# Kernel optimization log

Hardware: AMD Instinct MI355X
Metric: run time of the kernel (lower is better)

Reference implementation:

```python
import jax, jax.numpy as jnp
import numpy as np

N_VARS = 16
BATCH = 16
SEQ = 512
P = N_VARS * (N_VARS - 1)  # ordered pairs i != j


def setup_inputs() -> dict:
    key = jax.random.key(0)
    ks = jax.random.split(key, 12)
    n = N_VARS

    def w(k, shape, fan_in):
        return jax.random.normal(k, shape, dtype=jnp.float32) / np.sqrt(fan_in)

    z = lambda *s: jnp.zeros(s, jnp.float32)
    return {
        'data': jax.random.normal(ks[0], (BATCH, SEQ, n), dtype=jnp.float32),
        # structure learner: n*n -> 256 -> 128 -> n*n (dropout skipped / eval mode)
        'Ws1': w(ks[1], (n * n, 256), n * n), 'bs1': z(256),
        'Ws2': w(ks[2], (256, 128), 256), 'bs2': z(128),
        'Ws3': w(ks[3], (128, n * n), 128), 'bs3': z(n * n),
        # per-variable causal mechanisms (stacked): (n-1) -> 128 -> 64 -> 1
        'Wm1': w(ks[4], (n, n - 1, 128), n - 1), 'bm1': z(n, 128),
        'Wm2': w(ks[5], (n, 128, 64), 128), 'bm2': z(n, 64),
        'Wm3': w(ks[6], (n, 64), 64), 'bm3': z(n),
        # per-pair independence tests (stacked): 2 -> 32 -> 1, sigmoid
        'Wt1': w(ks[7], (P, 2, 32), 2), 'bt1': z(P, 32),
        'Wt2': w(ks[8], (P, 32), 32), 'bt2': z(P),
    }


def reference(data, Ws1, bs1, Ws2, bs2, Ws3, bs3,
              Wm1, bm1, Wm2, bm2, Wm3, bm3,
              Wt1, bt1, Wt2, bt2):
    B, S, n = data.shape
    N = B * S
    flat = data.reshape(N, n)  # [N, n] all samples

    # ---- correlations of batch-averaged series (vectorized corrcoef) ----
    avg = data.mean(axis=0)                    # [S, n]
    xc = avg - avg.mean(axis=0, keepdims=True)
    cov = xc.T @ xc                            # [n, n]
    std = jnp.sqrt(jnp.clip(jnp.diag(cov), 0.0))
    denom = std[:, None] * std[None, :]
    corr = jnp.abs(jnp.where(denom > 0, cov / jnp.where(denom > 0, denom, 1.0), 0.0))
    corr = corr * (1.0 - jnp.eye(n, dtype=corr.dtype))  # zero diagonal (i != j only)

    # ---- structure learner MLP -> sigmoid -> strict upper-tri DAG mask ----
    h = jax.nn.relu(corr.reshape(1, -1) @ Ws1 + bs1)
    h = jax.nn.relu(h @ Ws2 + bs2)
    adj = jax.nn.sigmoid(h @ Ws3 + bs3).reshape(n, n)
    adj = jnp.triu(adj, 1)

    # ---- causal mechanisms: gather-parents -> per-var MLP -> scatter ----
    idx = np.stack([[j for j in range(n) if j != v] for v in range(n)])  # [n, n-1]
    pmask = adj > 0.5
    parent_mask = pmask[idx, np.arange(n)[:, None]].astype(flat.dtype)   # [n, n-1]
    inp = flat[:, idx] * parent_mask[None]                               # [N, n, n-1]
    h1 = jax.nn.relu(jnp.einsum('nvp,vph->nvh', inp, Wm1) + bm1)         # [N, n, 128]
    h2 = jax.nn.relu(jnp.einsum('nvh,vhk->nvk', h1, Wm2) + bm2)          # [N, n, 64]
    mech = jnp.einsum('nvk,vk->nv', h2, Wm3) + bm3                       # [N, n]
    has_parents = parent_mask.sum(axis=1) > 0                            # [n]
    predictions = jnp.where(has_parents[None, :], mech, flat).reshape(B, S, n)

    # ---- batched per-pair independence tests ----
    pairs = np.array([(i, j) for i in range(n) for j in range(n) if i != j])
    pi, pj = pairs[:, 0], pairs[:, 1]
    X = jnp.stack([flat[:, pi], flat[:, pj]], axis=-1)                   # [N, P, 2]
    ht = jax.nn.relu(jnp.einsum('npc,pch->nph', X, Wt1) + bt1)           # [N, P, 32]
    s = jax.nn.sigmoid(jnp.einsum('nph,ph->np', ht, Wt2) + bt2).mean(axis=0)  # [P]
    scores = jnp.zeros((n, n), flat.dtype).at[pi, pj].set(s)

    return adj, predictions, scores
```

## Files before the change

### kernel.cpp

```cpp
#include <hip/hip_runtime.h>
#include <hip/hip_bf16.h>


typedef __attribute__((ext_vector_type(8))) short bf16x8;
typedef __attribute__((ext_vector_type(4))) short bf16x4;
typedef __attribute__((ext_vector_type(4))) float f32x4;

#define DEV __device__ __forceinline__
DEV short f2bf(float f){ __hip_bfloat16 h = __float2bfloat16(f); short s; __builtin_memcpy(&s,&h,2); return s; }
DEV float bf2f(short s){ __hip_bfloat16 h; __builtin_memcpy(&h,&s,2); return __bfloat162float(h); }

#define WS_P1(b)   ((b)*272)
#define WS_PM      8960
#define WS_HP      9200
#define WS_DUMMY   9400
#define WS_FLAG    9600
#define FLAG_MAGIC 0x1357F00D

__global__ void __launch_bounds__(512) k_main(
    const float* __restrict__ data,
    const float* __restrict__ Ws1, const float* __restrict__ bs1,
    const float* __restrict__ Ws2, const float* __restrict__ bs2,
    const float* __restrict__ Ws3, const float* __restrict__ bs3,
    const float* __restrict__ Wt1, const float* __restrict__ bt1,
    const float* __restrict__ Wt2, const float* __restrict__ bt2,
    float* __restrict__ wsf, float* __restrict__ out)
{
    __shared__ float sh[2048];
    __shared__ float av[16*17];
    int tid = threadIdx.x;
    int* flags = (int*)(wsf + WS_FLAG);

    if (blockIdx.x != 0) {
        int p = blockIdx.x - 1;

        if (blockIdx.x <= 32) {
            int b = blockIdx.x - 1;
            if (tid < 256) {
                int sl = tid >> 4, vv = tid & 15;
                int s = b*16 + sl;
                float acc = 0.f;
                #pragma unroll
                for (int bt = 0; bt < 16; ++bt) acc += data[bt*8192 + s*16 + vv];
                av[sl*17 + vv] = acc * (1.f/16.f);
            }
            __syncthreads();
            if (tid < 256) {
                int i = tid >> 4, j = tid & 15;
                float p1 = 0.f;
                #pragma unroll
                for (int r = 0; r < 16; ++r) p1 += av[r*17 + i] * av[r*17 + j];
                wsf[WS_P1(b) + tid] = p1;
            }
            if (tid < 16) {
                float ms = 0.f;
                #pragma unroll
                for (int r = 0; r < 16; ++r) ms += av[r*17 + tid];
                wsf[WS_P1(b) + 256 + tid] = ms;
            }
            __syncthreads();
            if (tid == 0) {
                __threadfence();
                __hip_atomic_store(&flags[b], FLAG_MAGIC,
                                   __ATOMIC_RELEASE, __HIP_MEMORY_SCOPE_AGENT);
            }
            unsigned xr = 0;
            { uint4 u = ((const uint4*)Ws1)[b*512 + tid]; xr ^= u.x^u.y^u.z^u.w; }
            if (tid < 256) { uint4 u = ((const uint4*)Ws2)[b*256 + tid];       xr ^= u.x^u.y^u.z^u.w; }
            else           { uint4 u = ((const uint4*)Ws3)[b*256 + tid - 256]; xr ^= u.x^u.y^u.z^u.w; }
            if (xr == 0x9E3779B9u) wsf[WS_DUMMY] = 0.f;
        }

        int i = p / 15, jr = p % 15;
        int j = jr + (jr >= i ? 1 : 0);
        float* w0 = sh;        float* w1 = sh + 32;
        float* bb = sh + 64;   float* w2 = sh + 96;
        float* red = sh + 128;
        if (tid < 32) {
            w0[tid] = Wt1[p*64 + tid];
            w1[tid] = Wt1[p*64 + 32 + tid];
            bb[tid] = bt1[p*32 + tid];
            w2[tid] = Wt2[p*32 + tid];
        }
        if (tid == 0) sh[700] = bt2[p];
        __syncthreads();
        float b2s = sh[700];
        float acc = 0.f;
        for (int it = 0; it < 16; ++it) {
            int s = it*512 + tid;
            float xa = data[s*16 + i];
            float xb = data[s*16 + j];
            float z = b2s;
            #pragma unroll
            for (int h = 0; h < 32; ++h) {
                float t1 = fmaf(xa, w0[h], fmaf(xb, w1[h], bb[h]));
                z = fmaf(fmaxf(t1, 0.f), w2[h], z);
            }
            acc += 1.f / (1.f + expf(-z));
        }
        red[tid] = acc;
        __syncthreads();
        for (int off = 256; off > 0; off >>= 1) {
            if (tid < off) red[tid] += red[tid + off];
            __syncthreads();
        }
        if (tid == 0) out[256 + 131072 + i*16 + j] = red[0] * (1.f/8192.f);
        return;
    }

    if (tid < 32) {
        while (__hip_atomic_load(&flags[tid], __ATOMIC_ACQUIRE,
                                 __HIP_MEMORY_SCOPE_AGENT) != FLAG_MAGIC)
            __builtin_amdgcn_s_sleep(8);
    }
    __syncthreads();
    __threadfence();

    float* corr_s = sh;          float* part   = sh + 256;
    float* h1_s   = sh + 768;    float* h2_s   = sh + 1024;
    float* adj_s  = sh + 1152;   float* pm_s   = sh + 1408;
    float* m_s    = sh + 1648;   float* std_s  = sh + 1664;
    float* cov_s  = sh + 1680;

    float p1 = 0.f;
    if (tid < 256) {
        #pragma unroll 8
        for (int b = 0; b < 32; ++b) p1 += wsf[WS_P1(b) + tid];
    }
    if (tid < 16) {
        float ms = 0.f;
        #pragma unroll 8
        for (int b = 0; b < 32; ++b) ms += wsf[WS_P1(b) + 256 + tid];
        m_s[tid] = ms * (1.f/512.f);
    }
    __syncthreads();
    if (tid < 256) { int i = tid>>4, j = tid&15; cov_s[tid] = p1 - 512.f*m_s[i]*m_s[j]; }
    __syncthreads();
    if (tid < 16) std_s[tid] = sqrtf(fmaxf(cov_s[tid*17], 0.f));
    __syncthreads();
    if (tid < 256) {
        int i = tid>>4, j = tid&15;
        float den = std_s[i]*std_s[j];
        corr_s[tid] = (den > 0.f && i != j) ? fabsf(cov_s[tid]/den) : 0.f;
    }
    __syncthreads();
    {
        int t = tid & 255, half = tid >> 8;
        const float* W1p = Ws1 + half*128*256;
        const float* cp  = corr_s + half*128;
        float a0=0.f, a1=0.f, a2=0.f, a3=0.f;
        #pragma unroll 8
        for (int i = 0; i < 128; i += 4) {
            a0 = fmaf(cp[i  ], W1p[(i  )*256 + t], a0);
            a1 = fmaf(cp[i+1], W1p[(i+1)*256 + t], a1);
            a2 = fmaf(cp[i+2], W1p[(i+2)*256 + t], a2);
            a3 = fmaf(cp[i+3], W1p[(i+3)*256 + t], a3);
        }
        part[half*256 + t] = a0+a1+a2+a3;
    }
    __syncthreads();
    if (tid < 256) h1_s[tid] = fmaxf(part[tid] + part[256 + tid] + bs1[tid], 0.f);
    __syncthreads();
    {
        int t = tid & 127, qq = tid >> 7;
        const float* W2p = Ws2 + qq*64*128;
        const float* h1p = h1_s + qq*64;
        float a0=0.f, a1=0.f, a2=0.f, a3=0.f;
        #pragma unroll 4
        for (int i = 0; i < 64; i += 4) {
            a0 = fmaf(h1p[i  ], W2p[(i  )*128 + t], a0);
            a1 = fmaf(h1p[i+1], W2p[(i+1)*128 + t], a1);
            a2 = fmaf(h1p[i+2], W2p[(i+2)*128 + t], a2);
            a3 = fmaf(h1p[i+3], W2p[(i+3)*128 + t], a3);
        }
        part[qq*128 + t] = a0+a1+a2+a3;
    }
    __syncthreads();
    if (tid < 128)
        h2_s[tid] = fmaxf(part[tid] + part[128+tid] + part[256+tid] + part[384+tid] + bs2[tid], 0.f);
    __syncthreads();
    {
        int t = tid & 255, half = tid >> 8;
        const float* W3p = Ws3 + half*64*256;
        const float* h2p = h2_s + half*64;
        float a0=0.f, a1=0.f, a2=0.f, a3=0.f;
        #pragma unroll 4
        for (int i = 0; i < 64; i += 4) {
            a0 = fmaf(h2p[i  ], W3p[(i  )*256 + t], a0);
            a1 = fmaf(h2p[i+1], W3p[(i+1)*256 + t], a1);
            a2 = fmaf(h2p[i+2], W3p[(i+2)*256 + t], a2);
            a3 = fmaf(h2p[i+3], W3p[(i+3)*256 + t], a3);
        }
        part[half*256 + t] = a0+a1+a2+a3;
    }
    __syncthreads();
    if (tid < 256) {
        float z = part[tid] + part[256 + tid] + bs3[tid];
        float a = 1.f / (1.f + expf(-z));
        int r = tid >> 4, cc = tid & 15;
        float adjv = (r < cc) ? a : 0.f;
        adj_s[tid] = adjv;
        out[tid] = adjv;
    }
    __syncthreads();
    if (tid < 240) {
        int v = tid / 15, pr = tid % 15;
        int jj = pr + (pr >= v ? 1 : 0);
        float pmv = (adj_s[jj*16 + v] > 0.5f) ? 1.f : 0.f;
        wsf[WS_PM + tid] = pmv;
        pm_s[tid] = pmv;
    }
    if (tid >= 256 && tid < 272) out[256 + 131072 + (tid-256)*17] = 0.f;
    __syncthreads();
    if (tid < 16) {
        float sum = 0.f;
        #pragma unroll
        for (int pr = 0; pr < 15; ++pr) sum += pm_s[tid*15 + pr];
        wsf[WS_HP + tid] = (sum > 0.f) ? 1.f : 0.f;
    }
}

__global__ void __launch_bounds__(256, 2) k_mech(
    const float* __restrict__ data,
    const float* __restrict__ Wm1, const float* __restrict__ bm1,
    const float* __restrict__ Wm2, const float* __restrict__ bm2,
    const float* __restrict__ Wm3, const float* __restrict__ bm3,
    const float* __restrict__ wsf, float* __restrict__ out)
{
    int tid = threadIdx.x, bid = blockIdx.x;
    int v = bid >> 5, chunk = bid & 31;
    int gs0 = chunk * 256;

    __shared__ __align__(16) short smX[256*24];
    __shared__ __align__(16) short smW2T[64*136];
    __shared__ __align__(16) short smH1[4][16*136];
    __shared__ __align__(16) float smW1[16*128];
    __shared__ __align__(16) float smB1[128];
    __shared__ float smB2[64];
    __shared__ float smW3[64];

    for (int e = tid; e < 2048; e += 256) {
        int k = e >> 7, h = e & 127;
        float val = 0.f;
        if (k != v) {
            int p = k - (k > v ? 1 : 0);
            val = Wm1[v*1920 + p*128 + h] * wsf[WS_PM + v*15 + p];
        }
        smW1[e] = val;
    }
    for (int e = tid; e < 8192; e += 256) {
        int h = e >> 6, j = e & 63;
        smW2T[j*136 + h] = f2bf(Wm2[v*8192 + e]);
    }
    for (int e = tid; e < 4096; e += 256) {
        int s = e >> 4, k = e & 15;
        smX[s*24 + k] = f2bf(data[gs0*16 + e]);
    }
    if (tid < 128) smB1[tid] = bm1[v*128 + tid];
    else if (tid < 192) smB2[tid - 128] = bm2[v*64 + tid - 128];
    else smW3[tid - 192] = Wm3[v*64 + tid - 192];
    __syncthreads();

    int lane = tid & 63, wid = tid >> 6;
    int c = lane & 15, q = lane >> 4;
    float hp = wsf[WS_HP + v];
    float bm3v = bm3[v];

    bf16x8 a1[8];
    #pragma unroll
    for (int ht = 0; ht < 8; ++ht) {
        #pragma unroll
        for (int jj = 0; jj < 8; ++jj) {
            int k = q*8 + jj;
            float w = (k < 16) ? smW1[k*128 + ht*16 + c] : 0.f;
            a1[ht][jj] = f2bf(w);
        }
    }
    bf16x8 b2r[16];
    #pragma unroll
    for (int jt = 0; jt < 4; ++jt)
        #pragma unroll
        for (int ks = 0; ks < 4; ++ks)
            b2r[jt*4 + ks] = *(const bf16x8*)&smW2T[(jt*16 + c)*136 + ks*32 + q*8];
    float w3c[4], b2c[4];
    #pragma unroll
    for (int jt = 0; jt < 4; ++jt) { w3c[jt] = smW3[jt*16 + c]; b2c[jt] = smB2[jt*16 + c]; }

    short* h1buf = smH1[wid];

    for (int stl = 0; stl < 4; ++stl) {
        int st = wid*4 + stl;
        bf16x8 xb;
        #pragma unroll
        for (int i2 = 0; i2 < 8; ++i2) xb[i2] = 0;
        if (q < 2) xb = *(const bf16x8*)&smX[(st*16 + c)*24 + q*8];
        f32x4 c1[8];
        #pragma unroll
        for (int ht = 0; ht < 8; ++ht) c1[ht] = *(const f32x4*)&smB1[ht*16 + q*4];
        #pragma unroll
        for (int ht = 0; ht < 8; ++ht)
            c1[ht] = __builtin_amdgcn_mfma_f32_16x16x32_bf16(a1[ht], xb, c1[ht], 0, 0, 0);
        #pragma unroll
        for (int ht = 0; ht < 8; ++ht) {
            bf16x4 pk;
            #pragma unroll
            for (int r = 0; r < 4; ++r) pk[r] = f2bf(fmaxf(c1[ht][r], 0.f));
            *(bf16x4*)&h1buf[c*136 + ht*16 + q*4] = pk;
        }
        f32x4 c2[4];
        #pragma unroll
        for (int jt = 0; jt < 4; ++jt) {
            float bi = b2c[jt];
            c2[jt] = (f32x4){bi, bi, bi, bi};
        }
        #pragma unroll
        for (int ks = 0; ks < 4; ++ks) {
            bf16x8 a2 = *(const bf16x8*)&h1buf[c*136 + ks*32 + q*8];
            #pragma unroll
            for (int jt = 0; jt < 4; ++jt)
                c2[jt] = __builtin_amdgcn_mfma_f32_16x16x32_bf16(a2, b2r[jt*4 + ks], c2[jt], 0, 0, 0);
        }
        float part[4];
        #pragma unroll
        for (int r = 0; r < 4; ++r) part[r] = 0.f;
        #pragma unroll
        for (int jt = 0; jt < 4; ++jt)
            #pragma unroll
            for (int r = 0; r < 4; ++r)
                part[r] = fmaf(fmaxf(c2[jt][r], 0.f), w3c[jt], part[r]);
        #pragma unroll
        for (int off = 1; off < 16; off <<= 1)
            #pragma unroll
            for (int r = 0; r < 4; ++r)
                part[r] += __shfl_xor(part[r], off, 16);
        if (c == 0) {
            #pragma unroll
            for (int r = 0; r < 4; ++r) {
                int s_loc = st*16 + q*4 + r;
                float mech = part[r] + bm3v;
                float xv = bf2f(smX[s_loc*24 + v]);
                out[256 + (gs0 + s_loc)*16 + v] = (hp != 0.f) ? mech : xv;
            }
        }
    }
}

extern "C" void kernel_launch(void* const* d_in, const int* in_sizes, int n_in,
                              void* d_out, int out_size, void* d_ws, size_t ws_size,
                              hipStream_t stream)
{
    const float* data = (const float*)d_in[0];
    const float* Ws1  = (const float*)d_in[1];
    const float* bs1  = (const float*)d_in[2];
    const float* Ws2  = (const float*)d_in[3];
    const float* bs2  = (const float*)d_in[4];
    const float* Ws3  = (const float*)d_in[5];
    const float* bs3  = (const float*)d_in[6];
    const float* Wm1  = (const float*)d_in[7];
    const float* bm1  = (const float*)d_in[8];
    const float* Wm2  = (const float*)d_in[9];
    const float* bm2  = (const float*)d_in[10];
    const float* Wm3  = (const float*)d_in[11];
    const float* bm3  = (const float*)d_in[12];
    const float* Wt1  = (const float*)d_in[13];
    const float* bt1  = (const float*)d_in[14];
    const float* Wt2  = (const float*)d_in[15];
    const float* bt2  = (const float*)d_in[16];
    float* wsf = (float*)d_ws;
    float* out = (float*)d_out;

    hipLaunchKernelGGL(k_main, dim3(241), dim3(512), 0, stream,
                       data, Ws1, bs1, Ws2, bs2, Ws3, bs3,
                       Wt1, bt1, Wt2, bt2, wsf, out);
    hipLaunchKernelGGL(k_mech, dim3(512), dim3(256), 0, stream,
                       data, Wm1, bm1, Wm2, bm2, Wm3, bm3, wsf, out);
}
```

Before: 120.8 us.

## Fuse graph, mechanism and pair kernels into one launch with redundant graph recompute

Merges the two launches into a single 496-block kernel. Each of the 256 mechanism blocks recomputes the full correlation and structure-learner MLP itself, so the cross-block flag spin-wait and the workspace round-trip go away. Mechanism blocks now process 512 samples each and read X directly from global memory instead of staging it in LDS. The cost is 256 redundant reads of the whole data tensor plus repeated small MLP work per block, in exchange for removing the second launch and the serialization on block 0.

```diff
diff --git a/kernel.cpp b/kernel.cpp
--- a/kernel.cpp
+++ b/kernel.cpp
@@ -10,270 +10,249 @@
 DEV short f2bf(float f){ __hip_bfloat16 h = __float2bfloat16(f); short s; __builtin_memcpy(&s,&h,2); return s; }
 DEV float bf2f(short s){ __hip_bfloat16 h; __builtin_memcpy(&h,&s,2); return __bfloat162float(h); }
 
-#define WS_P1(b)   ((b)*272)
-#define WS_PM      8960
-#define WS_HP      9200
-#define WS_DUMMY   9400
-#define WS_FLAG    9600
-#define FLAG_MAGIC 0x1357F00D
-
-__global__ void __launch_bounds__(512) k_main(
+struct GraphSm {
+    float avT[16 * 532];
+    float part[512];
+    float cov[256];
+    float corr[256];
+    float h1[256];
+    float h2[128];
+    float adj[256];
+    float m[16];
+    float stdv[16];
+};
+struct MechSm {
+    short W2T[64 * 136];
+    short H1[4][16 * 136];
+    float W1[16 * 128];
+    float B1[128];
+    float B2[64];
+    float W3[64];
+};
+struct PairSm {
+    float w0[32], w1[32], bb[32], w2[32];
+    float red[256];
+    float b2s;
+};
+union SmU { GraphSm g; MechSm m; PairSm p; };
+
+__global__ void __launch_bounds__(256, 2) k_fused(
     const float* __restrict__ data,
     const float* __restrict__ Ws1, const float* __restrict__ bs1,
     const float* __restrict__ Ws2, const float* __restrict__ bs2,
     const float* __restrict__ Ws3, const float* __restrict__ bs3,
+    const float* __restrict__ Wm1, const float* __restrict__ bm1,
+    const float* __restrict__ Wm2, const float* __restrict__ bm2,
+    const float* __restrict__ Wm3, const float* __restrict__ bm3,
     const float* __restrict__ Wt1, const float* __restrict__ bt1,
     const float* __restrict__ Wt2, const float* __restrict__ bt2,
-    float* __restrict__ wsf, float* __restrict__ out)
+    float* __restrict__ out)
 {
-    __shared__ float sh[2048];
-    __shared__ float av[16*17];
-    int tid = threadIdx.x;
-    int* flags = (int*)(wsf + WS_FLAG);
-
-    if (blockIdx.x != 0) {
-        int p = blockIdx.x - 1;
-
-        if (blockIdx.x <= 32) {
-            int b = blockIdx.x - 1;
-            if (tid < 256) {
-                int sl = tid >> 4, vv = tid & 15;
-                int s = b*16 + sl;
-                float acc = 0.f;
-                #pragma unroll
-                for (int bt = 0; bt < 16; ++bt) acc += data[bt*8192 + s*16 + vv];
-                av[sl*17 + vv] = acc * (1.f/16.f);
-            }
-            __syncthreads();
-            if (tid < 256) {
-                int i = tid >> 4, j = tid & 15;
-                float p1 = 0.f;
-                #pragma unroll
-                for (int r = 0; r < 16; ++r) p1 += av[r*17 + i] * av[r*17 + j];
-                wsf[WS_P1(b) + tid] = p1;
-            }
-            if (tid < 16) {
-                float ms = 0.f;
-                #pragma unroll
-                for (int r = 0; r < 16; ++r) ms += av[r*17 + tid];
-                wsf[WS_P1(b) + 256 + tid] = ms;
-            }
-            __syncthreads();
-            if (tid == 0) {
-                __threadfence();
-                __hip_atomic_store(&flags[b], FLAG_MAGIC,
-                                   __ATOMIC_RELEASE, __HIP_MEMORY_SCOPE_AGENT);
-            }
-            unsigned xr = 0;
-            { uint4 u = ((const uint4*)Ws1)[b*512 + tid]; xr ^= u.x^u.y^u.z^u.w; }
-            if (tid < 256) { uint4 u = ((const uint4*)Ws2)[b*256 + tid];       xr ^= u.x^u.y^u.z^u.w; }
-            else           { uint4 u = ((const uint4*)Ws3)[b*256 + tid - 256]; xr ^= u.x^u.y^u.z^u.w; }
-            if (xr == 0x9E3779B9u) wsf[WS_DUMMY] = 0.f;
-        }
-
+    __shared__ __align__(16) SmU sm;
+    __shared__ float pm_s[16];
+    __shared__ float hp_s;
+    int tid = threadIdx.x, bid = blockIdx.x;
+
+    if (bid >= 256) {
+        int p = bid - 256;
         int i = p / 15, jr = p % 15;
         int j = jr + (jr >= i ? 1 : 0);
-        float* w0 = sh;        float* w1 = sh + 32;
-        float* bb = sh + 64;   float* w2 = sh + 96;
-        float* red = sh + 128;
         if (tid < 32) {
-            w0[tid] = Wt1[p*64 + tid];
-            w1[tid] = Wt1[p*64 + 32 + tid];
-            bb[tid] = bt1[p*32 + tid];
-            w2[tid] = Wt2[p*32 + tid];
-        }
-        if (tid == 0) sh[700] = bt2[p];
+            sm.p.w0[tid] = Wt1[p*64 + tid];
+            sm.p.w1[tid] = Wt1[p*64 + 32 + tid];
+            sm.p.bb[tid] = bt1[p*32 + tid];
+            sm.p.w2[tid] = Wt2[p*32 + tid];
+        }
+        if (tid == 0) sm.p.b2s = bt2[p];
         __syncthreads();
-        float b2s = sh[700];
+        float b2sv = sm.p.b2s;
         float acc = 0.f;
-        for (int it = 0; it < 16; ++it) {
-            int s = it*512 + tid;
+        for (int it = 0; it < 32; ++it) {
+            int s = it*256 + tid;
             float xa = data[s*16 + i];
             float xb = data[s*16 + j];
-            float z = b2s;
+            float z = b2sv;
             #pragma unroll
             for (int h = 0; h < 32; ++h) {
-                float t1 = fmaf(xa, w0[h], fmaf(xb, w1[h], bb[h]));
-                z = fmaf(fmaxf(t1, 0.f), w2[h], z);
+                float t1 = fmaf(xa, sm.p.w0[h], fmaf(xb, sm.p.w1[h], sm.p.bb[h]));
+                z = fmaf(fmaxf(t1, 0.f), sm.p.w2[h], z);
             }
             acc += 1.f / (1.f + expf(-z));
         }
-        red[tid] = acc;
+        sm.p.red[tid] = acc;
         __syncthreads();
-        for (int off = 256; off > 0; off >>= 1) {
-            if (tid < off) red[tid] += red[tid + off];
+        for (int off = 128; off > 0; off >>= 1) {
+            if (tid < off) sm.p.red[tid] += sm.p.red[tid + off];
             __syncthreads();
         }
-        if (tid == 0) out[256 + 131072 + i*16 + j] = red[0] * (1.f/8192.f);
+        if (tid == 0) out[256 + 131072 + i*16 + j] = sm.p.red[0] * (1.f/8192.f);
         return;
     }
 
-    if (tid < 32) {
-        while (__hip_atomic_load(&flags[tid], __ATOMIC_ACQUIRE,
-                                 __HIP_MEMORY_SCOPE_AGENT) != FLAG_MAGIC)
-            __builtin_amdgcn_s_sleep(8);
-    }
-    __syncthreads();
-    __threadfence();
-
-    float* corr_s = sh;          float* part   = sh + 256;
-    float* h1_s   = sh + 768;    float* h2_s   = sh + 1024;
-    float* adj_s  = sh + 1152;   float* pm_s   = sh + 1408;
-    float* m_s    = sh + 1648;   float* std_s  = sh + 1664;
-    float* cov_s  = sh + 1680;
-
-    float p1 = 0.f;
-    if (tid < 256) {
-        #pragma unroll 8
-        for (int b = 0; b < 32; ++b) p1 += wsf[WS_P1(b) + tid];
-    }
+    int v = bid >> 4, chunk = bid & 15;
+    int gs0 = chunk * 512;
+
+    {
+        int vb = (tid & 3) * 4, sg = tid >> 2;
+        for (int k = 0; k < 8; ++k) {
+            int s = sg + k*64;
+            float ax=0.f, ay=0.f, az=0.f, aw=0.f;
+            #pragma unroll
+            for (int b = 0; b < 16; ++b) {
+                float4 d4 = *(const float4*)&data[b*8192 + s*16 + vb];
+                ax += d4.x; ay += d4.y; az += d4.z; aw += d4.w;
+            }
+            sm.g.avT[(vb+0)*532 + s] = ax * 0.0625f;
+            sm.g.avT[(vb+1)*532 + s] = ay * 0.0625f;
+            sm.g.avT[(vb+2)*532 + s] = az * 0.0625f;
+            sm.g.avT[(vb+3)*532 + s] = aw * 0.0625f;
+        }
+    }
+    __syncthreads();
+    if (tid < 128) {
+        int vv = tid >> 3, sgm = tid & 7;
+        const float* rp = &sm.g.avT[vv*532 + sgm*64];
+        float a0=0.f, a1=0.f, a2=0.f, a3=0.f;
+        for (int s = 0; s < 64; s += 4) {
+            float4 fa = *(const float4*)&rp[s];
+            a0 += fa.x; a1 += fa.y; a2 += fa.z; a3 += fa.w;
+        }
+        sm.g.part[tid] = (a0+a1)+(a2+a3);
+    }
+    __syncthreads();
     if (tid < 16) {
         float ms = 0.f;
-        #pragma unroll 8
-        for (int b = 0; b < 32; ++b) ms += wsf[WS_P1(b) + 256 + tid];
-        m_s[tid] = ms * (1.f/512.f);
-    }
-    __syncthreads();
-    if (tid < 256) { int i = tid>>4, j = tid&15; cov_s[tid] = p1 - 512.f*m_s[i]*m_s[j]; }
-    __syncthreads();
-    if (tid < 16) std_s[tid] = sqrtf(fmaxf(cov_s[tid*17], 0.f));
-    __syncthreads();
-    if (tid < 256) {
-        int i = tid>>4, j = tid&15;
-        float den = std_s[i]*std_s[j];
-        corr_s[tid] = (den > 0.f && i != j) ? fabsf(cov_s[tid]/den) : 0.f;
-    }
-    __syncthreads();
-    {
-        int t = tid & 255, half = tid >> 8;
-        const float* W1p = Ws1 + half*128*256;
-        const float* cp  = corr_s + half*128;
-        float a0=0.f, a1=0.f, a2=0.f, a3=0.f;
-        #pragma unroll 8
-        for (int i = 0; i < 128; i += 4) {
-            a0 = fmaf(cp[i  ], W1p[(i  )*256 + t], a0);
-            a1 = fmaf(cp[i+1], W1p[(i+1)*256 + t], a1);
-            a2 = fmaf(cp[i+2], W1p[(i+2)*256 + t], a2);
-            a3 = fmaf(cp[i+3], W1p[(i+3)*256 + t], a3);
-        }
-        part[half*256 + t] = a0+a1+a2+a3;
-    }
-    __syncthreads();
-    if (tid < 256) h1_s[tid] = fmaxf(part[tid] + part[256 + tid] + bs1[tid], 0.f);
-    __syncthreads();
-    {
-        int t = tid & 127, qq = tid >> 7;
-        const float* W2p = Ws2 + qq*64*128;
-        const float* h1p = h1_s + qq*64;
-        float a0=0.f, a1=0.f, a2=0.f, a3=0.f;
+        #pragma unroll
+        for (int q = 0; q < 8; ++q) ms += sm.g.part[tid*8 + q];
+        sm.g.m[tid] = ms * (1.f/512.f);
+    }
+    __syncthreads();
+    {
+        int ci = tid >> 4, cj = tid & 15;
+        int slo = (ci <= cj) ? 0   : 256;
+        int shi = (ci <  cj) ? 256 : 512;
+        const float* pi_ = &sm.g.avT[ci*532];
+        const float* pj_ = &sm.g.avT[cj*532];
+        float a0=0.f, a1=0.f, a2=0.f, a3=0.f;
+        for (int s = slo; s < shi; s += 4) {
+            float4 fa = *(const float4*)&pi_[s];
+            float4 fb = *(const float4*)&pj_[s];
+            a0 = fmaf(fa.x, fb.x, a0); a1 = fmaf(fa.y, fb.y, a1);
+            a2 = fmaf(fa.z, fb.z, a2); a3 = fmaf(fa.w, fb.w, a3);
+        }
+        sm.g.part[tid] = (a0+a1)+(a2+a3);
+    }
+    __syncthreads();
+    {
+        int ci = tid >> 4, cj = tid & 15;
+        float raw = (ci == cj) ? sm.g.part[tid]
+                               : sm.g.part[ci*16+cj] + sm.g.part[cj*16+ci];
+        sm.g.cov[tid] = raw - 512.f * sm.g.m[ci] * sm.g.m[cj];
+    }
+    __syncthreads();
+    if (tid < 16) sm.g.stdv[tid] = sqrtf(fmaxf(sm.g.cov[tid*17], 0.f));
+    __syncthreads();
+    {
+        int ci = tid >> 4, cj = tid & 15;
+        float den = sm.g.stdv[ci] * sm.g.stdv[cj];
+        sm.g.corr[tid] = (den > 0.f && ci != cj) ? fabsf(sm.g.cov[tid]/den) : 0.f;
+    }
+    __syncthreads();
+    {
+        float a0=0.f, a1=0.f, a2=0.f, a3=0.f;
+        const float* cp = sm.g.corr;
         #pragma unroll 4
-        for (int i = 0; i < 64; i += 4) {
-            a0 = fmaf(h1p[i  ], W2p[(i  )*128 + t], a0);
-            a1 = fmaf(h1p[i+1], W2p[(i+1)*128 + t], a1);
-            a2 = fmaf(h1p[i+2], W2p[(i+2)*128 + t], a2);
-            a3 = fmaf(h1p[i+3], W2p[(i+3)*128 + t], a3);
-        }
-        part[qq*128 + t] = a0+a1+a2+a3;
+        for (int k = 0; k < 256; k += 4) {
+            a0 = fmaf(cp[k  ], Ws1[(k  )*256 + tid], a0);
+            a1 = fmaf(cp[k+1], Ws1[(k+1)*256 + tid], a1);
+            a2 = fmaf(cp[k+2], Ws1[(k+2)*256 + tid], a2);
+            a3 = fmaf(cp[k+3], Ws1[(k+3)*256 + tid], a3);
+        }
+        sm.g.h1[tid] = fmaxf((a0+a1)+(a2+a3) + bs1[tid], 0.f);
+    }
+    __syncthreads();
+    {
+        int t = tid & 127, half = tid >> 7;
+        const float* h1p = sm.g.h1 + half*128;
+        const float* W2p = Ws2 + half*128*128;
+        float a0=0.f, a1=0.f, a2=0.f, a3=0.f;
+        #pragma unroll 4
+        for (int k = 0; k < 128; k += 4) {
+            a0 = fmaf(h1p[k  ], W2p[(k  )*128 + t], a0);
+            a1 = fmaf(h1p[k+1], W2p[(k+1)*128 + t], a1);
+            a2 = fmaf(h1p[k+2], W2p[(k+2)*128 + t], a2);
+            a3 = fmaf(h1p[k+3], W2p[(k+3)*128 + t], a3);
+        }
+        sm.g.part[tid] = (a0+a1)+(a2+a3);
     }
     __syncthreads();
     if (tid < 128)
-        h2_s[tid] = fmaxf(part[tid] + part[128+tid] + part[256+tid] + part[384+tid] + bs2[tid], 0.f);
-    __syncthreads();
-    {
-        int t = tid & 255, half = tid >> 8;
-        const float* W3p = Ws3 + half*64*256;
-        const float* h2p = h2_s + half*64;
-        float a0=0.f, a1=0.f, a2=0.f, a3=0.f;
+        sm.g.h2[tid] = fmaxf(sm.g.part[tid] + sm.g.part[128+tid] + bs2[tid], 0.f);
+    __syncthreads();
+    {
+        float a0=0.f, a1=0.f, a2=0.f, a3=0.f;
+        const float* h2p = sm.g.h2;
         #pragma unroll 4
-        for (int i = 0; i < 64; i += 4) {
-            a0 = fmaf(h2p[i  ], W3p[(i  )*256 + t], a0);
-            a1 = fmaf(h2p[i+1], W3p[(i+1)*256 + t], a1);
-            a2 = fmaf(h2p[i+2], W3p[(i+2)*256 + t], a2);
-            a3 = fmaf(h2p[i+3], W3p[(i+3)*256 + t], a3);
-        }
-        part[half*256 + t] = a0+a1+a2+a3;
-    }
-    __syncthreads();
-    if (tid < 256) {
-        float z = part[tid] + part[256 + tid] + bs3[tid];
+        for (int k = 0; k < 128; k += 4) {
+            a0 = fmaf(h2p[k  ], Ws3[(k  )*256 + tid], a0);
+            a1 = fmaf(h2p[k+1], Ws3[(k+1)*256 + tid], a1);
+            a2 = fmaf(h2p[k+2], Ws3[(k+2)*256 + tid], a2);
+            a3 = fmaf(h2p[k+3], Ws3[(k+3)*256 + tid], a3);
+        }
+        float z = (a0+a1)+(a2+a3) + bs3[tid];
         float a = 1.f / (1.f + expf(-z));
         int r = tid >> 4, cc = tid & 15;
         float adjv = (r < cc) ? a : 0.f;
-        adj_s[tid] = adjv;
-        out[tid] = adjv;
-    }
-    __syncthreads();
-    if (tid < 240) {
-        int v = tid / 15, pr = tid % 15;
-        int jj = pr + (pr >= v ? 1 : 0);
-        float pmv = (adj_s[jj*16 + v] > 0.5f) ? 1.f : 0.f;
-        wsf[WS_PM + tid] = pmv;
-        pm_s[tid] = pmv;
-    }
-    if (tid >= 256 && tid < 272) out[256 + 131072 + (tid-256)*17] = 0.f;
-    __syncthreads();
-    if (tid < 16) {
-        float sum = 0.f;
-        #pragma unroll
-        for (int pr = 0; pr < 15; ++pr) sum += pm_s[tid*15 + pr];
-        wsf[WS_HP + tid] = (sum > 0.f) ? 1.f : 0.f;
-    }
-}
-
-__global__ void __launch_bounds__(256, 2) k_mech(
-    const float* __restrict__ data,
-    const float* __restrict__ Wm1, const float* __restrict__ bm1,
-    const float* __restrict__ Wm2, const float* __restrict__ bm2,
-    const float* __restrict__ Wm3, const float* __restrict__ bm3,
-    const float* __restrict__ wsf, float* __restrict__ out)
-{
-    int tid = threadIdx.x, bid = blockIdx.x;
-    int v = bid >> 5, chunk = bid & 31;
-    int gs0 = chunk * 256;
-
-    __shared__ __align__(16) short smX[256*24];
-    __shared__ __align__(16) short smW2T[64*136];
-    __shared__ __align__(16) short smH1[4][16*136];
-    __shared__ __align__(16) float smW1[16*128];
-    __shared__ __align__(16) float smB1[128];
-    __shared__ float smB2[64];
-    __shared__ float smW3[64];
+        sm.g.adj[tid] = adjv;
+        if (bid == 0) out[tid] = adjv;
+    }
+    __syncthreads();
+    if (tid < 15) {
+        int jj = tid + (tid >= v ? 1 : 0);
+        pm_s[tid] = (sm.g.adj[jj*16 + v] > 0.5f) ? 1.f : 0.f;
+    }
+    if (bid == 0 && tid >= 16 && tid < 32)
+        out[256 + 131072 + (tid-16)*17] = 0.f;
+    __syncthreads();
+    if (tid == 0) {
+        float s = 0.f;
+        #pragma unroll
+        for (int pr = 0; pr < 15; ++pr) s += pm_s[pr];
+        hp_s = (s > 0.f) ? 1.f : 0.f;
+    }
+    __syncthreads();
 
     for (int e = tid; e < 2048; e += 256) {
         int k = e >> 7, h = e & 127;
         float val = 0.f;
         if (k != v) {
             int p = k - (k > v ? 1 : 0);
-            val = Wm1[v*1920 + p*128 + h] * wsf[WS_PM + v*15 + p];
-        }
-        smW1[e] = val;
+            val = Wm1[v*1920 + p*128 + h] * pm_s[p];
+        }
+        sm.m.W1[e] = val;
     }
     for (int e = tid; e < 8192; e += 256) {
-        int h = e >> 6, j = e & 63;
-        smW2T[j*136 + h] = f2bf(Wm2[v*8192 + e]);
-    }
-    for (int e = tid; e < 4096; e += 256) {
-        int s = e >> 4, k = e & 15;
-        smX[s*24 + k] = f2bf(data[gs0*16 + e]);
-    }
-    if (tid < 128) smB1[tid] = bm1[v*128 + tid];
-    else if (tid < 192) smB2[tid - 128] = bm2[v*64 + tid - 128];
-    else smW3[tid - 192] = Wm3[v*64 + tid - 192];
+        int h = e >> 6, jj2 = e & 63;
+        sm.m.W2T[jj2*136 + h] = f2bf(Wm2[v*8192 + e]);
+    }
+    if (tid < 128) sm.m.B1[tid] = bm1[v*128 + tid];
+    else if (tid < 192) sm.m.B2[tid - 128] = bm2[v*64 + tid - 128];
+    else sm.m.W3[tid - 192] = Wm3[v*64 + tid - 192];
     __syncthreads();
 
     int lane = tid & 63, wid = tid >> 6;
     int c = lane & 15, q = lane >> 4;
-    float hp = wsf[WS_HP + v];
+    float hp = hp_s;
     float bm3v = bm3[v];
 
-    bf16x8 a1[8];
+    bf16x8 a1f[8];
     #pragma unroll
     for (int ht = 0; ht < 8; ++ht) {
         #pragma unroll
         for (int jj = 0; jj < 8; ++jj) {
             int k = q*8 + jj;
-            float w = (k < 16) ? smW1[k*128 + ht*16 + c] : 0.f;
-            a1[ht][jj] = f2bf(w);
+            float w = (k < 16) ? sm.m.W1[k*128 + ht*16 + c] : 0.f;
+            a1f[ht][jj] = f2bf(w);
         }
     }
     bf16x8 b2r[16];
@@ -281,25 +260,33 @@
     for (int jt = 0; jt < 4; ++jt)
         #pragma unroll
         for (int ks = 0; ks < 4; ++ks)
-            b2r[jt*4 + ks] = *(const bf16x8*)&smW2T[(jt*16 + c)*136 + ks*32 + q*8];
+            b2r[jt*4 + ks] = *(const bf16x8*)&sm.m.W2T[(jt*16 + c)*136 + ks*32 + q*8];
     float w3c[4], b2c[4];
     #pragma unroll
-    for (int jt = 0; jt < 4; ++jt) { w3c[jt] = smW3[jt*16 + c]; b2c[jt] = smB2[jt*16 + c]; }
-
-    short* h1buf = smH1[wid];
-
-    for (int stl = 0; stl < 4; ++stl) {
-        int st = wid*4 + stl;
+    for (int jt = 0; jt < 4; ++jt) { w3c[jt] = sm.m.W3[jt*16 + c]; b2c[jt] = sm.m.B2[jt*16 + c]; }
+
+    short* h1buf = sm.m.H1[wid];
+
+    for (int stl = 0; stl < 8; ++stl) {
+        int st = wid*8 + stl;
         bf16x8 xb;
         #pragma unroll
         for (int i2 = 0; i2 < 8; ++i2) xb[i2] = 0;
-        if (q < 2) xb = *(const bf16x8*)&smX[(st*16 + c)*24 + q*8];
+        if (q < 2) {
+            const float* xp = &data[(gs0 + st*16 + c)*16 + q*8];
+            float4 u0 = *(const float4*)xp;
+            float4 u1 = *(const float4*)(xp + 4);
+            xb[0] = f2bf(u0.x); xb[1] = f2bf(u0.y);
+            xb[2] = f2bf(u0.z); xb[3] = f2bf(u0.w);
+            xb[4] = f2bf(u1.x); xb[5] = f2bf(u1.y);
+            xb[6] = f2bf(u1.z); xb[7] = f2bf(u1.w);
+        }
         f32x4 c1[8];
         #pragma unroll
-        for (int ht = 0; ht < 8; ++ht) c1[ht] = *(const f32x4*)&smB1[ht*16 + q*4];
+        for (int ht = 0; ht < 8; ++ht) c1[ht] = *(const f32x4*)&sm.m.B1[ht*16 + q*4];
         #pragma unroll
         for (int ht = 0; ht < 8; ++ht)
-            c1[ht] = __builtin_amdgcn_mfma_f32_16x16x32_bf16(a1[ht], xb, c1[ht], 0, 0, 0);
+            c1[ht] = __builtin_amdgcn_mfma_f32_16x16x32_bf16(a1f[ht], xb, c1[ht], 0, 0, 0);
         #pragma unroll
         for (int ht = 0; ht < 8; ++ht) {
             bf16x4 pk;
@@ -338,7 +325,7 @@
             for (int r = 0; r < 4; ++r) {
                 int s_loc = st*16 + q*4 + r;
                 float mech = part[r] + bm3v;
-                float xv = bf2f(smX[s_loc*24 + v]);
+                float xv = data[(gs0 + s_loc)*16 + v];
                 out[256 + (gs0 + s_loc)*16 + v] = (hp != 0.f) ? mech : xv;
             }
         }
@@ -366,12 +353,11 @@
     const float* bt1  = (const float*)d_in[14];
     const float* Wt2  = (const float*)d_in[15];
     const float* bt2  = (const float*)d_in[16];
-    float* wsf = (float*)d_ws;
     float* out = (float*)d_out;
-
-    hipLaunchKernelGGL(k_main, dim3(241), dim3(512), 0, stream,
+    (void)d_ws; (void)ws_size;
+
+    hipLaunchKernelGGL(k_fused, dim3(496), dim3(256), 0, stream,
                        data, Ws1, bs1, Ws2, bs2, Ws3, bs3,
-                       Wt1, bt1, Wt2, bt2, wsf, out);
-    hipLaunchKernelGGL(k_mech, dim3(512), dim3(256), 0, stream,
-                       data, Wm1, bm1, Wm2, bm2, Wm3, bm3, wsf, out);
+                       Wm1, bm1, Wm2, bm2, Wm3, bm3,
+                       Wt1, bt1, Wt2, bt2, out);
 }
```

New measurement: 130.4 us. 1.08x slower.
